# Performance work log

Measured on AMD Instinct MI355X. Metric: run time of the kernel, lower is better.

The kernel has to match this reference:

```python
import jax, jax.numpy as jnp
import numpy as np
import math

B, S, D, H = 2, 2048, 1024, 16
HD = D // H  # head dim = 64


def _rope_tables():
    # RoFormer sinusoidal position embedding: one frequency per (even, odd) pair
    pos = jnp.arange(S, dtype=jnp.float32)[:, None]                # [S, 1]
    inv_freq = 1.0 / (10000.0 ** (jnp.arange(0, HD, 2, dtype=jnp.float32) / HD))  # [HD/2]
    ang = pos * inv_freq[None, :]                                   # [S, HD/2]
    sin = jnp.sin(ang)[None, None]                                  # [1,1,S,HD/2]
    cos = jnp.cos(ang)[None, None]
    return sin, cos


def setup_inputs() -> dict:
    key = jax.random.key(0)
    k0, k1, k2, k3 = jax.random.split(key, 4)
    scale = 1.0 / math.sqrt(D)
    sin, cos = _rope_tables()
    return {
        "hidden_states": jax.random.normal(k0, (B, S, D), dtype=jnp.float32),
        "Wq": jax.random.normal(k1, (D, D), dtype=jnp.float32) * scale,
        "Wk": jax.random.normal(k2, (D, D), dtype=jnp.float32) * scale,
        "Wv": jax.random.normal(k3, (D, D), dtype=jnp.float32) * scale,
        "sin": sin,
        "cos": cos,
    }


def _split_heads(x):
    # [B,S,D] -> [B,H,S,HD]
    b, s, _ = x.shape
    return x.reshape(b, s, H, HD).transpose(0, 2, 1, 3)


def _apply_rotary(x, sin, cos):
    # x: [B,H,S,HD]; sin/cos broadcast as [1,1,S,HD/2]
    x1 = x[..., 0::2]
    x2 = x[..., 1::2]
    out = jnp.stack([x1 * cos - x2 * sin, x2 * cos + x1 * sin], axis=-1)
    return out.reshape(x.shape)


def reference(hidden_states, Wq, Wk, Wv, sin, cos):
    q = _apply_rotary(_split_heads(hidden_states @ Wq), sin, cos)  # [B,H,S,HD]
    k = _apply_rotary(_split_heads(hidden_states @ Wk), sin, cos)
    v = _apply_rotary(_split_heads(hidden_states @ Wv), sin, cos)  # note: RoPE on V too, per source
    scores = jnp.einsum("bhqd,bhkd->bhqk", q, k) / math.sqrt(HD)   # [B,H,S,S]
    probs = jax.nn.softmax(scores, axis=-1)
    ctx = jnp.einsum("bhqk,bhkd->bhqd", probs, v)                   # [B,H,S,HD]
    return ctx.transpose(0, 2, 1, 3).reshape(hidden_states.shape[0], S, D)
```

## Files before the change

kernel.cpp:

```cpp
#include <hip/hip_runtime.h>

typedef unsigned short u16;
typedef unsigned short u16x8 __attribute__((ext_vector_type(8)));
typedef unsigned short u16x4 __attribute__((ext_vector_type(4)));
typedef __bf16 bf16x8_t __attribute__((ext_vector_type(8)));
typedef float floatx4 __attribute__((ext_vector_type(4)));

#define BATCH 2
#define S_LEN 2048
#define D_DIM 1024
#define NH    16
#define HD    64

__device__ __forceinline__ u16 f2b(float f) {
  union { float f; unsigned int i; } c; c.f = f;
  const unsigned int i = c.i;
  return (u16)((i + 0x7FFFu + ((i >> 16) & 1u)) >> 16);
}
__device__ __forceinline__ unsigned int fbits(float f) {
  union { float f; unsigned int i; } c; c.f = f; return c.i;
}
__device__ __forceinline__ bf16x8_t asbf(u16x8 v) {
  union { u16x8 u; bf16x8_t b; } c; c.u = v; return c.b;
}
__device__ __forceinline__ void load_lds16(const u16* g, u16* l) {
  __builtin_amdgcn_global_load_lds(
      (const __attribute__((address_space(1))) void*)g,
      (__attribute__((address_space(3))) void*)l, 16, 0, 0);
}

__device__ __attribute__((aligned(256))) u16 g_xb[(size_t)BATCH * S_LEN * D_DIM];
__device__ __attribute__((aligned(256))) u16 g_wt[3u * D_DIM * D_DIM];
__device__ __attribute__((aligned(256))) u16 g_qkv[3u * BATCH * S_LEN * D_DIM];

__global__ __launch_bounds__(256) void prep(const float* __restrict__ X,
                                            const float* __restrict__ Wq,
                                            const float* __restrict__ Wk,
                                            const float* __restrict__ Wv) {
  const int tid = threadIdx.x;
  const int z = blockIdx.y;
  if (z == 3) {
#pragma unroll
    for (int c = 0; c < 8; ++c) {
      const size_t i = (((size_t)c * 256 + blockIdx.x) * 256 + tid) * 8;
      floatx4 a = *(const floatx4*)(X + i);
      floatx4 b = *(const floatx4*)(X + i + 4);
      u16x8 o;
#pragma unroll
      for (int j = 0; j < 4; ++j) { o[j] = f2b(a[j]); o[4 + j] = f2b(b[j]); }
      *(u16x8*)(g_xb + i) = o;
    }
    return;
  }
  __shared__ u16 t[64][65];
  const float* W = (z == 0) ? Wq : (z == 1) ? Wk : Wv;
  u16* Wt = g_wt + (size_t)z * D_DIM * D_DIM;
  const int k0 = (blockIdx.x & 15) * 64;
  const int n0 = (blockIdx.x >> 4) * 64;
  const int rr = tid >> 4;
  const int cc = (tid & 15) * 4;
#pragma unroll
  for (int i = 0; i < 4; ++i) {
    const int r = rr + i * 16;
    floatx4 v = *(const floatx4*)(W + (size_t)(k0 + r) * D_DIM + n0 + cc);
    t[r][cc] = f2b(v[0]); t[r][cc + 1] = f2b(v[1]);
    t[r][cc + 2] = f2b(v[2]); t[r][cc + 3] = f2b(v[3]);
  }
  __syncthreads();
#pragma unroll
  for (int i = 0; i < 4; ++i) {
    const int r = rr + i * 16;
    u16x4 v;
    v[0] = t[cc][r]; v[1] = t[cc + 1][r]; v[2] = t[cc + 2][r]; v[3] = t[cc + 3][r];
    *(u16x4*)(Wt + (size_t)(n0 + r) * D_DIM + k0 + cc) = v;
  }
}

__global__ __launch_bounds__(256) void qkv_gemm(const float* __restrict__ sin_t,
                                                const float* __restrict__ cos_t) {
  __shared__ __attribute__((aligned(16))) u16 lds_a[128 * 32];
  __shared__ __attribute__((aligned(16))) u16 lds_b[128 * 32];
  const int tid = threadIdx.x;
  const int wv = tid >> 6;
  const int lane = tid & 63;
  const int lrow = lane & 15;
  const int quad = lane >> 4;
  const int wr = wv >> 1, wc = wv & 1;
  const int m0 = blockIdx.x * 128;
  const int n0 = blockIdx.y * 128;
  const int z = blockIdx.z;
  const bool vmode = (z == 2);
  const u16* Wz = g_wt + (size_t)z * (D_DIM * D_DIM);

  floatx4 acc[4][4] = {};

  const int srow = lane >> 2;
  const int scol = (lane & 3) * 8;
  const u16* gA = g_xb + (size_t)(m0 + wv * 32 + srow) * D_DIM + scol;
  const u16* gB = Wz   + (size_t)(n0 + wv * 32 + srow) * D_DIM + scol;
  u16* sA = &lds_a[(wv * 32) * 32];
  u16* sB = &lds_b[(wv * 32) * 32];

  const u16* Aarr = vmode ? lds_b : lds_a;
  const u16* Barr = vmode ? lds_a : lds_b;

  for (int k0 = 0; k0 < D_DIM; k0 += 32) {
    __syncthreads();
    load_lds16(gA + k0, sA);
    load_lds16(gA + (size_t)16 * D_DIM + k0, sA + 512);
    load_lds16(gB + k0, sB);
    load_lds16(gB + (size_t)16 * D_DIM + k0, sB + 512);
    __syncthreads();
    u16x8 af[4], bfr[4];
#pragma unroll
    for (int mi = 0; mi < 4; ++mi)
      af[mi] = *(const u16x8*)&Aarr[(wr * 64 + mi * 16 + lrow) * 32 + quad * 8];
#pragma unroll
    for (int ni = 0; ni < 4; ++ni)
      bfr[ni] = *(const u16x8*)&Barr[(wc * 64 + ni * 16 + lrow) * 32 + quad * 8];
#pragma unroll
    for (int mi = 0; mi < 4; ++mi)
#pragma unroll
      for (int ni = 0; ni < 4; ++ni)
        acc[mi][ni] = __builtin_amdgcn_mfma_f32_16x16x32_bf16(
            asbf(af[mi]), asbf(bfr[ni]), acc[mi][ni], 0, 0, 0);
  }

  if (!vmode) {
    u16* outz = g_qkv + (size_t)z * (BATCH * S_LEN * D_DIM);
#pragma unroll
    for (int mi = 0; mi < 4; ++mi) {
      const int m = m0 + wr * 64 + mi * 16 + quad * 4;
      const int b = m >> 11;
#pragma unroll
      for (int ni = 0; ni < 4; ++ni) {
        const int n = n0 + wc * 64 + ni * 16 + lrow;
        const int h = n >> 6, hd = n & 63;
        const int i0 = hd >> 1;
        const float sgn = (hd & 1) ? 1.f : -1.f;
        u16* op = outz + (((size_t)(b * NH + h) * S_LEN + (m & 2047)) * HD + hd);
#pragma unroll
        for (int r = 0; r < 4; ++r) {
          const int s = (m + r) & 2047;
          const float c  = cos_t[(size_t)s * 32 + i0];
          const float sn = sin_t[(size_t)s * 32 + i0];
          const float v = acc[mi][ni][r];
          const float vp = __shfl_xor(v, 1);
          op[r * HD] = f2b(v * c + sgn * sn * vp);
        }
      }
    }
  } else {
    u16* outv = g_qkv + (size_t)2 * (BATCH * S_LEN * D_DIM);
#pragma unroll
    for (int mi = 0; mi < 4; ++mi) {
      const int hb = n0 + wr * 64 + mi * 16 + quad * 4;
#pragma unroll
      for (int ni = 0; ni < 4; ++ni) {
        const int sg = m0 + wc * 64 + ni * 16 + lrow;
        const int b = sg >> 11, s = sg & 2047;
#pragma unroll
        for (int r = 0; r < 4; ++r) {
          const int hdg = hb + r;
          const int h = (hdg >> 6) & 15, hd = hdg & 63;
          const float c  = cos_t[(size_t)s * 32 + (hd >> 1)];
          const float sn = sin_t[(size_t)s * 32 + (hd >> 1)];
          const float v  = acc[mi][ni][r];
          const float vp = acc[mi][ni][r ^ 1];
          const float val = (r & 1) ? (v * c + sn * vp) : (v * c - sn * vp);
          outv[((size_t)(b * NH + h) * HD + hd) * S_LEN + s] = f2b(val);
        }
      }
    }
  }
}

__global__ __launch_bounds__(256) void flash_attn(float* __restrict__ out) {
  __shared__ __attribute__((aligned(16))) u16 lds_k[64 * 72];
  __shared__ __attribute__((aligned(16))) u16 lds_v[64 * 72];
  __shared__ __attribute__((aligned(16))) u16 lds_p[4][16 * 72];
  const int bh = blockIdx.x;
  const int qt = blockIdx.y;
  const int b = bh >> 4, h = bh & 15;
  const int tid = threadIdx.x, wv = tid >> 6, lane = tid & 63;
  const int lrow = lane & 15, quad = lane >> 4;
  const u16* Qb  = g_qkv + (size_t)bh * (S_LEN * HD);
  const u16* Kb  = g_qkv + (size_t)(BATCH * NH + bh) * (S_LEN * HD);
  const u16* VTb = g_qkv + (size_t)(2 * BATCH * NH + bh) * (S_LEN * HD);
  const int q0 = qt * 64 + wv * 16;

  u16x8 qf[2];
#pragma unroll
  for (int ks = 0; ks < 2; ++ks)
    qf[ks] = *(const u16x8*)(Qb + (size_t)(q0 + lrow) * HD + ks * 32 + quad * 8);

  floatx4 oacc[4] = {};
  float l_part = 0.f;
  const float cexp = 0.125f * 1.44269504088896f;

  const int sr = tid >> 3;
  const int sc = (tid & 7) * 8;
  u16* lp = lds_p[wv];

  for (int t = 0; t < S_LEN / 64; ++t) {
    const int kv0 = t * 64;
#pragma unroll
    for (int i = 0; i < 2; ++i) {
      const int r = sr + i * 32;
      *(u16x8*)&lds_k[r * 72 + sc] =
          *(const u16x8*)(Kb + (size_t)(kv0 + r) * HD + sc);
      *(u16x8*)&lds_v[r * 72 + sc] =
          *(const u16x8*)(VTb + (size_t)r * S_LEN + kv0 + sc);
    }
    __syncthreads();

    floatx4 sacc[4] = {};
#pragma unroll
    for (int nb = 0; nb < 4; ++nb)
#pragma unroll
      for (int ks = 0; ks < 2; ++ks) {
        u16x8 kf = *(const u16x8*)&lds_k[(nb * 16 + lrow) * 72 + ks * 32 + quad * 8];
        sacc[nb] = __builtin_amdgcn_mfma_f32_16x16x32_bf16(
            asbf(kf), asbf(qf[ks]), sacc[nb], 0, 0, 0);
      }

#pragma unroll
    for (int nb = 0; nb < 4; ++nb) {
      float p0 = exp2f(sacc[nb][0] * cexp);
      float p1 = exp2f(sacc[nb][1] * cexp);
      float p2 = exp2f(sacc[nb][2] * cexp);
      float p3 = exp2f(sacc[nb][3] * cexp);
      l_part += (p0 + p1) + (p2 + p3);
      uint2 pk;
      pk.x = __byte_perm(fbits(p0), fbits(p1), 0x7632);
      pk.y = __byte_perm(fbits(p2), fbits(p3), 0x7632);
      *(uint2*)&lp[lrow * 72 + nb * 16 + quad * 4] = pk;
    }

#pragma unroll
    for (int ks = 0; ks < 2; ++ks) {
      u16x8 pf = *(const u16x8*)&lp[lrow * 72 + ks * 32 + quad * 8];
#pragma unroll
      for (int hb = 0; hb < 4; ++hb) {
        u16x8 vf = *(const u16x8*)&lds_v[(hb * 16 + lrow) * 72 + ks * 32 + quad * 8];
        oacc[hb] = __builtin_amdgcn_mfma_f32_16x16x32_bf16(
            asbf(pf), asbf(vf), oacc[hb], 0, 0, 0);
      }
    }
    __syncthreads();
  }

  float l = l_part;
  l += __shfl_xor(l, 16);
  l += __shfl_xor(l, 32);
  float linv[4];
#pragma unroll
  for (int r = 0; r < 4; ++r)
    linv[r] = 1.f / __shfl(l, quad * 4 + r);

#pragma unroll
  for (int hb = 0; hb < 4; ++hb) {
    const int hd = hb * 16 + lrow;
#pragma unroll
    for (int r = 0; r < 4; ++r) {
      const int q = q0 + quad * 4 + r;
      out[((size_t)(b * S_LEN) + q) * D_DIM + h * HD + hd] = oacc[hb][r] * linv[r];
    }
  }
}

extern "C" void kernel_launch(void* const* d_in, const int* in_sizes, int n_in,
                              void* d_out, int out_size, void* d_ws, size_t ws_size,
                              hipStream_t stream) {
  const float* X = (const float*)d_in[0];
  const float* sin_t = (const float*)d_in[4];
  const float* cos_t = (const float*)d_in[5];

  prep<<<dim3(256, 4), 256, 0, stream>>>(X, (const float*)d_in[1],
                                         (const float*)d_in[2],
                                         (const float*)d_in[3]);

  qkv_gemm<<<dim3(32, 8, 3), 256, 0, stream>>>(sin_t, cos_t);

  flash_attn<<<dim3(32, 32), 256, 0, stream>>>((float*)d_out);
}
```

Measured before the change: 212.7 us.

## Double-buffer K/V tiles in flash attention and fold softmax scale into Q

The attention kernel now prefetches the next K/V tile into registers and writes it into alternating LDS buffers, so global loads overlap compute and one barrier per iteration is removed. The softmax scale and log2(e) factor are folded into Q during the projection epilogue, which lets the inner loop use the raw hardware exp2. The QKV GEMM swaps operand roles so the Q/K epilogue writes four contiguous bf16 values per store and the V-transposed epilogue writes vectorised along the sequence. The cost is more LDS and registers, and the rotary pairing and sign handling in the epilogue were rewritten.

Measured after the change: 196.9 us. -7.4%, faster.

```diff
diff --git a/kernel.cpp b/kernel.cpp
--- a/kernel.cpp
+++ b/kernel.cpp
@@ -94,15 +94,13 @@
 
   floatx4 acc[4][4] = {};
 
-  const int srow = lane >> 2;
-  const int scol = (lane & 3) * 8;
-  const u16* gA = g_xb + (size_t)(m0 + wv * 32 + srow) * D_DIM + scol;
-  const u16* gB = Wz   + (size_t)(n0 + wv * 32 + srow) * D_DIM + scol;
+  const u16* gA = g_xb + (size_t)(m0 + wv * 32 + (lane >> 2)) * D_DIM + (lane & 3) * 8;
+  const u16* gB = Wz   + (size_t)(n0 + wv * 32 + (lane >> 2)) * D_DIM + (lane & 3) * 8;
   u16* sA = &lds_a[(wv * 32) * 32];
   u16* sB = &lds_b[(wv * 32) * 32];
 
-  const u16* Aarr = vmode ? lds_b : lds_a;
-  const u16* Barr = vmode ? lds_a : lds_b;
+  const u16* Aarr = vmode ? lds_a : lds_b;
+  const u16* Barr = vmode ? lds_b : lds_a;
 
   for (int k0 = 0; k0 < D_DIM; k0 += 32) {
     __syncthreads();
@@ -127,57 +125,60 @@
   }
 
   if (!vmode) {
+    const float qsc = (z == 0) ? 0.18033688011112042f : 1.0f;
     u16* outz = g_qkv + (size_t)z * (BATCH * S_LEN * D_DIM);
 #pragma unroll
     for (int mi = 0; mi < 4; ++mi) {
-      const int m = m0 + wr * 64 + mi * 16 + quad * 4;
-      const int b = m >> 11;
+      const int nf0 = n0 + wr * 64 + mi * 16 + quad * 4;
+      const int h = nf0 >> 6, hd0 = nf0 & 63, i00 = hd0 >> 1;
 #pragma unroll
       for (int ni = 0; ni < 4; ++ni) {
-        const int n = n0 + wc * 64 + ni * 16 + lrow;
-        const int h = n >> 6, hd = n & 63;
-        const int i0 = hd >> 1;
+        const int sg = m0 + wc * 64 + ni * 16 + lrow;
+        const int b = sg >> 11, srow = sg & 2047;
+        const float c0 = cos_t[(size_t)srow * 32 + i00];
+        const float s0 = sin_t[(size_t)srow * 32 + i00];
+        const float c1 = cos_t[(size_t)srow * 32 + i00 + 1];
+        const float s1 = sin_t[(size_t)srow * 32 + i00 + 1];
+        const float v0 = acc[mi][ni][0], v1 = acc[mi][ni][1];
+        const float v2 = acc[mi][ni][2], v3 = acc[mi][ni][3];
+        u16x4 ov;
+        ov[0] = f2b((v0 * c0 - v1 * s0) * qsc);
+        ov[1] = f2b((v1 * c0 + v0 * s0) * qsc);
+        ov[2] = f2b((v2 * c1 - v3 * s1) * qsc);
+        ov[3] = f2b((v3 * c1 + v2 * s1) * qsc);
+        *(u16x4*)(outz + ((size_t)(b * NH + h) * S_LEN + srow) * HD + hd0) = ov;
+      }
+    }
+  } else {
+    u16* outv = g_qkv + (size_t)2 * (BATCH * S_LEN * D_DIM);
+#pragma unroll
+    for (int mi = 0; mi < 4; ++mi) {
+      const int s0g = m0 + wr * 64 + mi * 16 + quad * 4;
+      const int b = s0g >> 11, sl = s0g & 2047;
+#pragma unroll
+      for (int ni = 0; ni < 4; ++ni) {
+        const int nf = n0 + wc * 64 + ni * 16 + lrow;
+        const int h = nf >> 6, hd = nf & 63, i0 = hd >> 1;
         const float sgn = (hd & 1) ? 1.f : -1.f;
-        u16* op = outz + (((size_t)(b * NH + h) * S_LEN + (m & 2047)) * HD + hd);
+        u16x4 ov;
 #pragma unroll
         for (int r = 0; r < 4; ++r) {
-          const int s = (m + r) & 2047;
+          const int s = sl + r;
           const float c  = cos_t[(size_t)s * 32 + i0];
           const float sn = sin_t[(size_t)s * 32 + i0];
-          const float v = acc[mi][ni][r];
+          const float v  = acc[mi][ni][r];
           const float vp = __shfl_xor(v, 1);
-          op[r * HD] = f2b(v * c + sgn * sn * vp);
+          ov[r] = f2b(v * c + sgn * sn * vp);
         }
-      }
-    }
-  } else {
-    u16* outv = g_qkv + (size_t)2 * (BATCH * S_LEN * D_DIM);
-#pragma unroll
-    for (int mi = 0; mi < 4; ++mi) {
-      const int hb = n0 + wr * 64 + mi * 16 + quad * 4;
-#pragma unroll
-      for (int ni = 0; ni < 4; ++ni) {
-        const int sg = m0 + wc * 64 + ni * 16 + lrow;
-        const int b = sg >> 11, s = sg & 2047;
-#pragma unroll
-        for (int r = 0; r < 4; ++r) {
-          const int hdg = hb + r;
-          const int h = (hdg >> 6) & 15, hd = hdg & 63;
-          const float c  = cos_t[(size_t)s * 32 + (hd >> 1)];
-          const float sn = sin_t[(size_t)s * 32 + (hd >> 1)];
-          const float v  = acc[mi][ni][r];
-          const float vp = acc[mi][ni][r ^ 1];
-          const float val = (r & 1) ? (v * c + sn * vp) : (v * c - sn * vp);
-          outv[((size_t)(b * NH + h) * HD + hd) * S_LEN + s] = f2b(val);
-        }
+        *(u16x4*)(outv + ((size_t)(b * NH + h) * HD + hd) * S_LEN + sl) = ov;
       }
     }
   }
 }
 
 __global__ __launch_bounds__(256) void flash_attn(float* __restrict__ out) {
-  __shared__ __attribute__((aligned(16))) u16 lds_k[64 * 72];
-  __shared__ __attribute__((aligned(16))) u16 lds_v[64 * 72];
+  __shared__ __attribute__((aligned(16))) u16 lds_k[2][64 * 72];
+  __shared__ __attribute__((aligned(16))) u16 lds_v[2][64 * 72];
   __shared__ __attribute__((aligned(16))) u16 lds_p[4][16 * 72];
   const int bh = blockIdx.x;
   const int qt = blockIdx.y;
@@ -196,40 +197,54 @@
 
   floatx4 oacc[4] = {};
   float l_part = 0.f;
-  const float cexp = 0.125f * 1.44269504088896f;
 
   const int sr = tid >> 3;
   const int sc = (tid & 7) * 8;
   u16* lp = lds_p[wv];
 
+  u16x8 kreg[2], vreg[2];
+#pragma unroll
+  for (int i = 0; i < 2; ++i) {
+    const int r = sr + i * 32;
+    kreg[i] = *(const u16x8*)(Kb + (size_t)r * HD + sc);
+    vreg[i] = *(const u16x8*)(VTb + (size_t)r * S_LEN + sc);
+  }
+
   for (int t = 0; t < S_LEN / 64; ++t) {
-    const int kv0 = t * 64;
+    const int buf = t & 1;
 #pragma unroll
     for (int i = 0; i < 2; ++i) {
       const int r = sr + i * 32;
-      *(u16x8*)&lds_k[r * 72 + sc] =
-          *(const u16x8*)(Kb + (size_t)(kv0 + r) * HD + sc);
-      *(u16x8*)&lds_v[r * 72 + sc] =
-          *(const u16x8*)(VTb + (size_t)r * S_LEN + kv0 + sc);
+      *(u16x8*)&lds_k[buf][r * 72 + sc] = kreg[i];
+      *(u16x8*)&lds_v[buf][r * 72 + sc] = vreg[i];
     }
     __syncthreads();
+    if (t + 1 < S_LEN / 64) {
+      const int kv0n = (t + 1) * 64;
+#pragma unroll
+      for (int i = 0; i < 2; ++i) {
+        const int r = sr + i * 32;
+        kreg[i] = *(const u16x8*)(Kb + (size_t)(kv0n + r) * HD + sc);
+        vreg[i] = *(const u16x8*)(VTb + (size_t)r * S_LEN + kv0n + sc);
+      }
+    }
 
     floatx4 sacc[4] = {};
 #pragma unroll
     for (int nb = 0; nb < 4; ++nb)
 #pragma unroll
       for (int ks = 0; ks < 2; ++ks) {
-        u16x8 kf = *(const u16x8*)&lds_k[(nb * 16 + lrow) * 72 + ks * 32 + quad * 8];
+        u16x8 kf = *(const u16x8*)&lds_k[buf][(nb * 16 + lrow) * 72 + ks * 32 + quad * 8];
         sacc[nb] = __builtin_amdgcn_mfma_f32_16x16x32_bf16(
             asbf(kf), asbf(qf[ks]), sacc[nb], 0, 0, 0);
       }
 
 #pragma unroll
     for (int nb = 0; nb < 4; ++nb) {
-      float p0 = exp2f(sacc[nb][0] * cexp);
-      float p1 = exp2f(sacc[nb][1] * cexp);
-      float p2 = exp2f(sacc[nb][2] * cexp);
-      float p3 = exp2f(sacc[nb][3] * cexp);
+      const float p0 = __builtin_amdgcn_exp2f(sacc[nb][0]);
+      const float p1 = __builtin_amdgcn_exp2f(sacc[nb][1]);
+      const float p2 = __builtin_amdgcn_exp2f(sacc[nb][2]);
+      const float p3 = __builtin_amdgcn_exp2f(sacc[nb][3]);
       l_part += (p0 + p1) + (p2 + p3);
       uint2 pk;
       pk.x = __byte_perm(fbits(p0), fbits(p1), 0x7632);
@@ -242,12 +257,11 @@
       u16x8 pf = *(const u16x8*)&lp[lrow * 72 + ks * 32 + quad * 8];
 #pragma unroll
       for (int hb = 0; hb < 4; ++hb) {
-        u16x8 vf = *(const u16x8*)&lds_v[(hb * 16 + lrow) * 72 + ks * 32 + quad * 8];
+        u16x8 vf = *(const u16x8*)&lds_v[buf][(hb * 16 + lrow) * 72 + ks * 32 + quad * 8];
         oacc[hb] = __builtin_amdgcn_mfma_f32_16x16x32_bf16(
             asbf(pf), asbf(vf), oacc[hb], 0, 0, 0);
       }
     }
-    __syncthreads();
   }
 
   float l = l_part;
```
